# Kernel optimization log

Measured on AMD Instinct MI355X. Metric: run time of the kernel, lower is better.

Reference implementation:

```python
import jax, jax.numpy as jnp
import numpy as np

N_HEADS = 6
N_KV_HEADS = 2
HEAD_DIM = 128
REPEATS = N_HEADS // N_KV_HEADS  # 3


def setup_inputs() -> dict:
    key = jax.random.key(0)
    ks = jax.random.split(key, 5)
    B, S, D = 2, 4096, 768
    std = 1.0 / np.sqrt(D)
    return {
        "x": jax.random.normal(ks[0], (B, S, D), dtype=jnp.float32),
        "wq": jax.random.normal(ks[1], (D, N_HEADS * HEAD_DIM), dtype=jnp.float32) * std,
        "wk": jax.random.normal(ks[2], (D, N_KV_HEADS * HEAD_DIM), dtype=jnp.float32) * std,
        "wv": jax.random.normal(ks[3], (D, N_KV_HEADS * HEAD_DIM), dtype=jnp.float32) * std,
        "wo": jax.random.normal(ks[4], (N_HEADS * HEAD_DIM, D), dtype=jnp.float32) * std,
    }


def reference(x, wq, wk, wv, wo):
    B, S, _ = x.shape
    # projections
    q = (x @ wq).reshape(B, S, N_HEADS, HEAD_DIM)
    k = (x @ wk).reshape(B, S, N_KV_HEADS, HEAD_DIM)
    v = (x @ wv).reshape(B, S, N_KV_HEADS, HEAD_DIM)
    # GQA: repeat kv heads (repeat_interleave along head axis)
    k = jnp.repeat(k, REPEATS, axis=2)  # [B,S,H,D]
    v = jnp.repeat(v, REPEATS, axis=2)
    scale = 1.0 / jnp.sqrt(jnp.asarray(HEAD_DIM, x.dtype))
    # full bidirectional attention, [B,H,S,S] scores
    attn = jnp.einsum("bqhd,bkhd->bhqk", q * scale, k)
    attn = jax.nn.softmax(attn, axis=-1)
    out = jnp.einsum("bhqk,bkhd->bqhd", attn, v).reshape(B, S, N_HEADS * HEAD_DIM)
    return out @ wo
```

## Files before the change

### kernel.cpp

```cpp
#include <hip/hip_runtime.h>


typedef __attribute__((ext_vector_type(8))) short bf16x8;
typedef __attribute__((ext_vector_type(4))) float floatx4;
typedef __attribute__((ext_vector_type(4))) unsigned short ushort4v;

#define MFMA16(a, b, c) __builtin_amdgcn_mfma_f32_16x16x32_bf16((a), (b), (c), 0, 0, 0)

#if __has_builtin(__builtin_amdgcn_exp2f)
#define EXP2F(x) __builtin_amdgcn_exp2f(x)
#else
#define EXP2F(x) exp2f(x)
#endif

#define GLOAD_LDS16(gptr, lptr)                                                   \
  __builtin_amdgcn_global_load_lds(                                               \
      (const __attribute__((address_space(1))) unsigned int*)(gptr),              \
      (__attribute__((address_space(3))) unsigned int*)(lptr), 16, 0, 0)

__device__ __forceinline__ unsigned short f2bf(float f) {
  unsigned int u = __builtin_bit_cast(unsigned int, f);
  u = u + 0x7FFFu + ((u >> 16) & 1u);
  return (unsigned short)(u >> 16);
}

__device__ __forceinline__ unsigned short f2bf_fast(float f) {
  unsigned int u = __builtin_bit_cast(unsigned int, f);
  return (unsigned short)((u + 0x8000u) >> 16);
}

__device__ __forceinline__ float bf2f(unsigned short v) {
  return __builtin_bit_cast(float, (unsigned int)v << 16);
}


__global__ __launch_bounds__(256) void k_cvt_x(const float* __restrict__ x,
                                               unsigned short* __restrict__ xb, int n) {
  int i = (blockIdx.x * 256 + threadIdx.x) * 4;
  if (i + 3 < n) {
    float4 v = *(const float4*)(x + i);
    xb[i + 0] = f2bf(v.x);
    xb[i + 1] = f2bf(v.y);
    xb[i + 2] = f2bf(v.z);
    xb[i + 3] = f2bf(v.w);
  }
}

__global__ __launch_bounds__(256) void k_cvt_wqkv(const float* __restrict__ wq,
                                                  const float* __restrict__ wk,
                                                  const float* __restrict__ wv,
                                                  unsigned short* __restrict__ wt) {
  const float QSCALE = 1.4426950408889634f * 0.08838834764831843f;
  int idx = blockIdx.x * 256 + threadIdx.x;
  int n = idx / 768, k = idx - n * 768;
  float v;
  if (n < 768)       v = wq[k * 768 + n] * QSCALE;
  else if (n < 1024) v = wk[k * 256 + (n - 768)];
  else               v = wv[k * 256 + (n - 1024)];
  wt[idx] = f2bf(v);
}

__global__ __launch_bounds__(256) void k_cvt_wo(const float* __restrict__ wo,
                                                unsigned short* __restrict__ wt) {
  int idx = blockIdx.x * 256 + threadIdx.x;
  int n = idx / 768, k = idx - n * 768;
  wt[idx] = f2bf(wo[k * 768 + n]);
}


__device__ __forceinline__ void store_out(float* C, int i, float v) { C[i] = v; }
__device__ __forceinline__ void store_out(unsigned short* C, int i, float v) { C[i] = f2bf(v); }

template <typename OUT_T, bool SPLIT_V>
__global__ __launch_bounds__(256) void k_gemm(const unsigned short* __restrict__ A, int lda,
                                              const unsigned short* __restrict__ Bt, int ldb,
                                              OUT_T* __restrict__ C, int ldc, int K,
                                              unsigned short* __restrict__ vTout) {
  __shared__ __align__(16) unsigned short As[128 * 40];
  __shared__ __align__(16) unsigned short Bs[128 * 40];
  const int tid = threadIdx.x;
  const int wave = tid >> 6, lane = tid & 63;
  const int quad = lane >> 4, l16 = lane & 15;
  const int wm = (wave >> 1) * 64, wn = (wave & 1) * 64;
  const int m0 = blockIdx.y * 128, n0 = blockIdx.x * 128;

  floatx4 acc[4][4] = {};
  const int srow = tid >> 2;
  const int sseg = (tid & 3) * 8;

  for (int k0 = 0; k0 < K; k0 += 32) {
    __syncthreads();
#pragma unroll
    for (int h = 0; h < 2; h++) {
      int r = srow + h * 64;
      *(uint4*)(&As[r * 40 + sseg]) = *(const uint4*)(&A[(m0 + r) * lda + k0 + sseg]);
      *(uint4*)(&Bs[r * 40 + sseg]) = *(const uint4*)(&Bt[(n0 + r) * ldb + k0 + sseg]);
    }
    __syncthreads();

    bf16x8 af[4], bfr[4];
#pragma unroll
    for (int mf = 0; mf < 4; mf++)
      af[mf] = *(const bf16x8*)(&As[(wm + mf * 16 + l16) * 40 + quad * 8]);
#pragma unroll
    for (int nf = 0; nf < 4; nf++)
      bfr[nf] = *(const bf16x8*)(&Bs[(wn + nf * 16 + l16) * 40 + quad * 8]);
#pragma unroll
    for (int mf = 0; mf < 4; mf++)
#pragma unroll
      for (int nf = 0; nf < 4; nf++)
        acc[mf][nf] = MFMA16(af[mf], bfr[nf], acc[mf][nf]);
  }

#pragma unroll
  for (int mf = 0; mf < 4; mf++)
#pragma unroll
    for (int nf = 0; nf < 4; nf++) {
      int col = n0 + wn + nf * 16 + l16;
      if (SPLIT_V && col >= 1024) {
        int cc = col - 1024;
        int kvhh = cc >> 7, d = cc & 127;
        int row0 = m0 + wm + mf * 16 + quad * 4;
        int bb = row0 >> 12, s = row0 & 4095;
        ushort4v pv;
        pv.x = f2bf(acc[mf][nf][0]);
        pv.y = f2bf(acc[mf][nf][1]);
        pv.z = f2bf(acc[mf][nf][2]);
        pv.w = f2bf(acc[mf][nf][3]);
        *(ushort4v*)(&vTout[((size_t)((bb * 2 + kvhh) * 128) + d) * 4096 + s]) = pv;
      } else {
#pragma unroll
        for (int r = 0; r < 4; r++) {
          int row = m0 + wm + mf * 16 + quad * 4 + r;
          store_out(C, row * ldc + col, acc[mf][nf][r]);
        }
      }
    }
}


#define NSEG 4

#define KS_OFF(row, c) (((row) << 7) + ((((c) ^ ((row) & 7))) << 3))
#define VS_OFF(row, c) (((row) << 6) + ((((c) ^ ((row) & 7))) << 3))

__global__ __launch_bounds__(256) void k_attn(const unsigned short* __restrict__ qkv,
                                              const unsigned short* __restrict__ vT,
                                              unsigned short* __restrict__ Opart,
                                              float* __restrict__ lpart) {
  __shared__ __align__(16) unsigned short Ks[64 * 128];
  __shared__ __align__(16) unsigned short Vt[128 * 64];
  __shared__ __align__(16) unsigned short Ps[128 * 64];

  const int qt = blockIdx.x, h = blockIdx.y;
  const int seg = blockIdx.z >> 1, b = blockIdx.z & 1;
  const int kvh = h / 3;
  const int tid = threadIdx.x, w = tid >> 6, lane = tid & 63;
  const int quad = lane >> 4, l16 = lane & 15;

  const char* qbase = (const char*)(qkv + (size_t)(b * 4096) * 1280 + h * 128);
  const char* kbase = (const char*)(qkv + (size_t)(b * 4096) * 1280 + 768 + kvh * 128);
  const char* vtb   = (const char*)(vT + (size_t)((b * 2 + kvh) * 128) * 4096);

  bf16x8 qf[2][4];
  floatx4 acc[2][8] = {};
  float l_i[2] = {0.f, 0.f};

#pragma unroll
  for (int it = 0; it < 8; it++) {
    int cb = it * 256 + w * 64;
    int j = cb + lane;
    int r = j >> 4, c = (j & 15) ^ (r & 7);
    unsigned short* dst = (cb < 1024) ? &Ks[cb * 8] : &Vt[(cb - 1024) * 8];
    GLOAD_LDS16(qbase + (size_t)(qt * 128 + r) * 2560 + c * 16, dst);
  }
  __syncthreads();

  {
    const unsigned short* qsrc = (w < 2) ? Ks : Vt;
    const int qr0 = (w & 1) * 32;
#pragma unroll
    for (int qg = 0; qg < 2; qg++)
#pragma unroll
      for (int dc = 0; dc < 4; dc++)
        qf[qg][dc] = *(const bf16x8*)(&qsrc[KS_OFF(qr0 + qg * 16 + l16, dc * 4 + quad)]);
  }
  __syncthreads();

  auto stage_k = [&](int kt) {
#pragma unroll
    for (int it = 0; it < 4; it++) {
      int cb = it * 256 + w * 64;
      int j = cb + lane;
      int r = j >> 4, c = (j & 15) ^ (r & 7);
      GLOAD_LDS16(kbase + (size_t)(kt * 64 + r) * 2560 + c * 16, &Ks[cb * 8]);
    }
  };
  auto stage_v = [&](int kt) {
#pragma unroll
    for (int it = 0; it < 4; it++) {
      int cb = it * 256 + w * 64;
      int j = cb + lane;
      int r = j >> 3, c = (j & 7) ^ (r & 7);
      GLOAD_LDS16(vtb + (size_t)r * 8192 + kt * 128 + c * 16, &Vt[cb * 8]);
    }
  };

  const int k0 = seg * 16;
  stage_k(k0);

#pragma unroll 1
  for (int i = 0; i < 16; i++) {
    __syncthreads();
    stage_v(k0 + i);

    floatx4 sfr[2][4] = {};
#pragma unroll
    for (int nf = 0; nf < 4; nf++)
#pragma unroll
      for (int dc = 0; dc < 4; dc++) {
        bf16x8 kf = *(const bf16x8*)(&Ks[KS_OFF(nf * 16 + l16, dc * 4 + quad)]);
        sfr[0][nf] = MFMA16(kf, qf[0][dc], sfr[0][nf]);
        sfr[1][nf] = MFMA16(kf, qf[1][dc], sfr[1][nf]);
      }

#pragma unroll
    for (int qg = 0; qg < 2; qg++) {
      float rs = 0.f;
#pragma unroll
      for (int nf = 0; nf < 4; nf++) {
#pragma unroll
        for (int r = 0; r < 4; r++) {
          float p = EXP2F(sfr[qg][nf][r]);
          sfr[qg][nf][r] = p;
          rs += p;
        }
        int row = w * 32 + qg * 16 + l16;
        int ch = nf * 2 + (quad >> 1);
        ushort4v pw;
        pw.x = f2bf_fast(sfr[qg][nf][0]);
        pw.y = f2bf_fast(sfr[qg][nf][1]);
        pw.z = f2bf_fast(sfr[qg][nf][2]);
        pw.w = f2bf_fast(sfr[qg][nf][3]);
        *(ushort4v*)(&Ps[VS_OFF(row, ch) + (quad & 1) * 4]) = pw;
      }
      rs += __shfl_xor(rs, 16, 64);
      rs += __shfl_xor(rs, 32, 64);
      l_i[qg] += rs;
    }

    __syncthreads();
    if (i < 15) stage_k(k0 + i + 1);

#pragma unroll
    for (int kc = 0; kc < 2; kc++) {
      bf16x8 pf0 = *(const bf16x8*)(&Ps[VS_OFF(w * 32 + l16, kc * 4 + quad)]);
      bf16x8 pf1 = *(const bf16x8*)(&Ps[VS_OFF(w * 32 + 16 + l16, kc * 4 + quad)]);
#pragma unroll
      for (int df = 0; df < 8; df++) {
        bf16x8 vf = *(const bf16x8*)(&Vt[VS_OFF(df * 16 + l16, kc * 4 + quad)]);
        acc[0][df] = MFMA16(pf0, vf, acc[0][df]);
        acc[1][df] = MFMA16(pf1, vf, acc[1][df]);
      }
    }
  }

#pragma unroll
  for (int qg = 0; qg < 2; qg++) {
    if (quad == 0)
      lpart[((size_t)(seg * 2 + b) * 6 + h) * 4096 + qt * 128 + w * 32 + qg * 16 + l16] = l_i[qg];
#pragma unroll
    for (int r = 0; r < 4; r++) {
      int row = qt * 128 + w * 32 + qg * 16 + quad * 4 + r;
      unsigned short* orow =
          Opart + (size_t)seg * 8192 * 768 + (size_t)(b * 4096 + row) * 768 + h * 128;
#pragma unroll
      for (int df = 0; df < 8; df++)
        orow[df * 16 + l16] = f2bf_fast(acc[qg][df][r]);
    }
  }
}

__global__ __launch_bounds__(256) void k_reduce(const unsigned short* __restrict__ Opart,
                                                const float* __restrict__ lpart,
                                                unsigned short* __restrict__ ob) {
  int idx = (blockIdx.x * 256 + threadIdx.x) * 4;
  int row = idx / 768, col = idx - row * 768;
  int h = col >> 7;
  int b = row >> 12, r = row & 4095;

  float lt = 0.f;
#pragma unroll
  for (int s = 0; s < NSEG; s++)
    lt += lpart[((size_t)(s * 2 + b) * 6 + h) * 4096 + r];
  float inv = 1.0f / lt;

  float acc0 = 0.f, acc1 = 0.f, acc2 = 0.f, acc3 = 0.f;
#pragma unroll
  for (int s = 0; s < NSEG; s++) {
    ushort4v v = *(const ushort4v*)(&Opart[(size_t)s * 8192 * 768 + idx]);
    acc0 += bf2f(v.x);
    acc1 += bf2f(v.y);
    acc2 += bf2f(v.z);
    acc3 += bf2f(v.w);
  }
  ushort4v o;
  o.x = f2bf(acc0 * inv);
  o.y = f2bf(acc1 * inv);
  o.z = f2bf(acc2 * inv);
  o.w = f2bf(acc3 * inv);
  *(ushort4v*)(&ob[idx]) = o;
}


extern "C" void kernel_launch(void* const* d_in, const int* in_sizes, int n_in,
                              void* d_out, int out_size, void* d_ws, size_t ws_size,
                              hipStream_t stream) {
  const float* x  = (const float*)d_in[0];
  const float* wq = (const float*)d_in[1];
  const float* wk = (const float*)d_in[2];
  const float* wv = (const float*)d_in[3];
  const float* wo = (const float*)d_in[4];
  float* out = (float*)d_out;

  char* ws = (char*)d_ws;
  unsigned short* xb    = (unsigned short*)(ws);
  unsigned short* wqkvT = (unsigned short*)(ws + 12582912);
  unsigned short* woT   = (unsigned short*)(ws + 14548992);
  unsigned short* qkvb  = (unsigned short*)(ws + 15728640);
  unsigned short* ob    = (unsigned short*)(ws + 36700160);
  unsigned short* Opart = (unsigned short*)(ws + 49283072);
  float*          lpart = (float*)(ws + 99614720);
  unsigned short* vT    = ob;

  k_cvt_x<<<6144, 256, 0, stream>>>(x, xb, 8192 * 768);
  k_cvt_wqkv<<<3840, 256, 0, stream>>>(wq, wk, wv, wqkvT);
  k_cvt_wo<<<2304, 256, 0, stream>>>(wo, woT);

  k_gemm<unsigned short, true><<<dim3(10, 64), 256, 0, stream>>>(
      xb, 768, wqkvT, 768, qkvb, 1280, 768, vT);

  k_attn<<<dim3(32, 6, 2 * NSEG), 256, 0, stream>>>(qkvb, vT, Opart, lpart);

  k_reduce<<<6144, 256, 0, stream>>>(Opart, lpart, ob);

  k_gemm<float, false><<<dim3(6, 64), 256, 0, stream>>>(ob, 768, woT, 768, out, 768, 768, nullptr);
}
```

Baseline: 275.8 us.

## Double-buffer GEMM with direct global-to-LDS loads and fuse weight transposes

The projection GEMMs now stage A/B tiles with global_load_lds into two swizzled LDS buffers, so the next k-slice loads while the current one feeds MFMAs. The old synchronous register round-trip with padded LDS is removed. The separate uncoalesced weight transpose kernels are merged into one tiled shared-memory transpose kernel. This relies on the barrier waiting for the async LDS loads, and the swizzle must match between writes and reads.

```diff
diff --git a/kernel.cpp b/kernel.cpp
--- a/kernel.cpp
+++ b/kernel.cpp
@@ -46,25 +46,40 @@
   }
 }
 
-__global__ __launch_bounds__(256) void k_cvt_wqkv(const float* __restrict__ wq,
-                                                  const float* __restrict__ wk,
-                                                  const float* __restrict__ wv,
-                                                  unsigned short* __restrict__ wt) {
+__global__ __launch_bounds__(256) void k_cvt_w(const float* __restrict__ wq,
+                                               const float* __restrict__ wk,
+                                               const float* __restrict__ wv,
+                                               const float* __restrict__ wo,
+                                               unsigned short* __restrict__ wqkvT,
+                                               unsigned short* __restrict__ woT) {
+  __shared__ float T[64 * 65];
   const float QSCALE = 1.4426950408889634f * 0.08838834764831843f;
-  int idx = blockIdx.x * 256 + threadIdx.x;
-  int n = idx / 768, k = idx - n * 768;
-  float v;
-  if (n < 768)       v = wq[k * 768 + n] * QSCALE;
-  else if (n < 1024) v = wk[k * 256 + (n - 768)];
-  else               v = wv[k * 256 + (n - 1024)];
-  wt[idx] = f2bf(v);
-}
-
-__global__ __launch_bounds__(256) void k_cvt_wo(const float* __restrict__ wo,
-                                                unsigned short* __restrict__ wt) {
-  int idx = blockIdx.x * 256 + threadIdx.x;
-  int n = idx / 768, k = idx - n * 768;
-  wt[idx] = f2bf(wo[k * 768 + n]);
+  const int kb = blockIdx.x, nb = blockIdx.y, tid = threadIdx.x;
+
+  const float* src; int ld, col0; unsigned short* dst; int n0; float scale = 1.0f;
+  if (nb < 12)      { src = wq; ld = 768; col0 = nb * 64;        dst = wqkvT; n0 = nb * 64; scale = QSCALE; }
+  else if (nb < 16) { src = wk; ld = 256; col0 = (nb - 12) * 64; dst = wqkvT; n0 = nb * 64; }
+  else if (nb < 20) { src = wv; ld = 256; col0 = (nb - 16) * 64; dst = wqkvT; n0 = nb * 64; }
+  else              { src = wo; ld = 768; col0 = (nb - 20) * 64; dst = woT;   n0 = (nb - 20) * 64; }
+
+  const int k0 = kb * 64;
+  {
+    int cc = tid & 63, kk0 = tid >> 6;
+#pragma unroll
+    for (int it = 0; it < 16; it++) {
+      int kk = kk0 + it * 4;
+      T[kk * 65 + cc] = src[(size_t)(k0 + kk) * ld + col0 + cc] * scale;
+    }
+  }
+  __syncthreads();
+  {
+    int kk = tid & 63, nn0 = tid >> 6;
+#pragma unroll
+    for (int it = 0; it < 16; it++) {
+      int nn = nn0 + it * 4;
+      dst[(size_t)(n0 + nn) * 768 + k0 + kk] = f2bf(T[kk * 65 + nn]);
+    }
+  }
 }
 
 
@@ -76,8 +91,11 @@
                                               const unsigned short* __restrict__ Bt, int ldb,
                                               OUT_T* __restrict__ C, int ldc, int K,
                                               unsigned short* __restrict__ vTout) {
-  __shared__ __align__(16) unsigned short As[128 * 40];
-  __shared__ __align__(16) unsigned short Bs[128 * 40];
+  __shared__ __align__(16) unsigned short As0[128 * 32];
+  __shared__ __align__(16) unsigned short As1[128 * 32];
+  __shared__ __align__(16) unsigned short Bs0[128 * 32];
+  __shared__ __align__(16) unsigned short Bs1[128 * 32];
+
   const int tid = threadIdx.x;
   const int wave = tid >> 6, lane = tid & 63;
   const int quad = lane >> 4, l16 = lane & 15;
@@ -85,31 +103,48 @@
   const int m0 = blockIdx.y * 128, n0 = blockIdx.x * 128;
 
   floatx4 acc[4][4] = {};
-  const int srow = tid >> 2;
-  const int sseg = (tid & 3) * 8;
-
-  for (int k0 = 0; k0 < K; k0 += 32) {
-    __syncthreads();
-#pragma unroll
-    for (int h = 0; h < 2; h++) {
-      int r = srow + h * 64;
-      *(uint4*)(&As[r * 40 + sseg]) = *(const uint4*)(&A[(m0 + r) * lda + k0 + sseg]);
-      *(uint4*)(&Bs[r * 40 + sseg]) = *(const uint4*)(&Bt[(n0 + r) * ldb + k0 + sseg]);
-    }
-    __syncthreads();
-
+
+  auto stage = [&](const unsigned short* G, int ld, int row0, int k0, unsigned short* S) {
+#pragma unroll
+    for (int it = 0; it < 2; it++) {
+      int j = it * 256 + tid;
+      int r = j >> 2, c = (j & 3) ^ (r & 3);
+      GLOAD_LDS16((const char*)(G + (size_t)(row0 + r) * ld + k0 + c * 8), &S[j * 8]);
+    }
+  };
+
+  const int xq = (quad ^ (l16 & 3)) * 8;
+  auto compute = [&](const unsigned short* As, const unsigned short* Bs) {
     bf16x8 af[4], bfr[4];
 #pragma unroll
     for (int mf = 0; mf < 4; mf++)
-      af[mf] = *(const bf16x8*)(&As[(wm + mf * 16 + l16) * 40 + quad * 8]);
+      af[mf] = *(const bf16x8*)(&As[(wm + mf * 16 + l16) * 32 + xq]);
 #pragma unroll
     for (int nf = 0; nf < 4; nf++)
-      bfr[nf] = *(const bf16x8*)(&Bs[(wn + nf * 16 + l16) * 40 + quad * 8]);
+      bfr[nf] = *(const bf16x8*)(&Bs[(wn + nf * 16 + l16) * 32 + xq]);
 #pragma unroll
     for (int mf = 0; mf < 4; mf++)
 #pragma unroll
       for (int nf = 0; nf < 4; nf++)
         acc[mf][nf] = MFMA16(af[mf], bfr[nf], acc[mf][nf]);
+  };
+
+  stage(A, lda, m0, 0, As0);
+  stage(Bt, ldb, n0, 0, Bs0);
+
+  const int half = K >> 6;
+#pragma unroll 1
+  for (int i = 0; i < half; i++) {
+    __syncthreads();
+    stage(A, lda, m0, (2 * i + 1) * 32, As1);
+    stage(Bt, ldb, n0, (2 * i + 1) * 32, Bs1);
+    compute(As0, Bs0);
+    __syncthreads();
+    if (i < half - 1) {
+      stage(A, lda, m0, (2 * i + 2) * 32, As0);
+      stage(Bt, ldb, n0, (2 * i + 2) * 32, Bs0);
+    }
+    compute(As1, Bs1);
   }
 
 #pragma unroll
@@ -334,8 +369,7 @@
   unsigned short* vT    = ob;
 
   k_cvt_x<<<6144, 256, 0, stream>>>(x, xb, 8192 * 768);
-  k_cvt_wqkv<<<3840, 256, 0, stream>>>(wq, wk, wv, wqkvT);
-  k_cvt_wo<<<2304, 256, 0, stream>>>(wo, woT);
+  k_cvt_w<<<dim3(12, 32), 256, 0, stream>>>(wq, wk, wv, wo, wqkvT, woT);
 
   k_gemm<unsigned short, true><<<dim3(10, 64), 256, 0, stream>>>(
       xb, 768, wqkvT, 768, qkvb, 1280, 768, vT);
```

After: 255.6 us. 1.08x faster.
